# Kernel tuning notes

Measured on AMD Instinct MI355X. Metric: run time of the kernel, lower is better.

The kernel has to match this reference:

```python
import jax, jax.numpy as jnp
import numpy as np

N = 500_000          # nodes
E = 8_000_000        # edges (avg degree 16)
C = 2                # in/out channels
STEP_DIM = 8
NUM_STEPS = 100
K = 2                # k_hops -> powers [0, 1]
HID = 8              # hidden_layers


def setup_inputs() -> dict:
    key = jax.random.key(0)
    ks = jax.random.split(key, 6)
    X = jax.random.normal(ks[0], (N, C), dtype=jnp.float32)
    edge_index = jax.random.randint(ks[1], (2, E), 0, N, dtype=jnp.int32)
    step_emb = jax.random.normal(ks[2], (NUM_STEPS, STEP_DIM), dtype=jnp.float32)
    d_in0 = C + STEP_DIM  # 10
    # layer 0: one Linear per power p in {0,1}
    W0 = jax.random.normal(ks[3], (K, d_in0, C), dtype=jnp.float32) / np.sqrt(d_in0).astype(np.float32)
    b0 = jnp.zeros((K, C), dtype=jnp.float32)
    # layers 1..7, stacked for lax.scan
    Wh = jax.random.normal(ks[4], (HID - 1, K, C, C), dtype=jnp.float32) / np.sqrt(C).astype(np.float32)
    bh = jnp.zeros((HID - 1, K, C), dtype=jnp.float32)
    return dict(X=X, edge_index=edge_index, step_index=7, step_emb=step_emb,
                W0=W0, b0=b0, Wh=Wh, bh=bh)


def _make_prop(edge_index, n):
    """GCN-normalized propagation with self-loops (PyG gcn_norm), as used by MixHopConv."""
    src, dst = edge_index[0], edge_index[1]
    # in-degree on destination nodes, +1 for the self-loop
    deg = jnp.zeros((n,), jnp.float32).at[dst].add(1.0) + 1.0
    dis = jax.lax.rsqrt(deg)  # deg^{-1/2}; deg >= 1 so no inf handling needed
    edge_w = dis[src] * dis[dst]  # [E]

    def prop(x):
        msg = x[src] * edge_w[:, None]                      # [E, F] gather
        out = jax.ops.segment_sum(msg, dst, num_segments=n)  # [N, F] scatter-add
        return out + x * (dis * dis)[:, None]               # self-loop term
    return prop


def reference(X, edge_index, step_index, step_emb, W0, b0, Wh, bh):
    n = X.shape[0]
    prop = _make_prop(edge_index, n)

    s = jnp.broadcast_to(step_emb[step_index], (n, STEP_DIM))
    x = jnp.concatenate([X, s], axis=-1)  # [N, 10]

    # layer 0: concat(xW0, (Ax)W1) -> view(-1,K,C).sum(1) -> relu  ==  relu(xW0+b0 + (Ax)W1+b1)
    x = jax.nn.relu(x @ W0[0] + b0[0] + prop(x) @ W0[1] + b0[1])  # [N, 2]

    def body(x, wb):
        W, b = wb  # W: [K, C, C], b: [K, C]
        h = x @ W[0] + b[0] + prop(x) @ W[1] + b[1]
        return jax.nn.relu(h), None

    x, _ = jax.lax.scan(body, x, (Wh, bh))
    return x
```

## Files before the change

kernel.cpp:

```cpp
#include <hip/hip_runtime.h>


constexpr int NN = 500000;
constexpr int NE = 8000000;
constexpr int STEP_DIM = 8;
constexpr int HIDM1 = 7;

constexpr int BSH  = 9;
constexpr int BNOD = 1 << BSH;
constexpr int NBUK = (NN + BNOD - 1) / BNOD;
constexpr int NQ   = 4;
constexpr int SUBQ = 2560;
constexpr int SLOT = NQ * SUBQ;
constexpr int KEYS = NQ * BNOD;
constexpr unsigned SENT = (unsigned)BNOD << 19;

constexpr int PA_NBLK = 500;
constexpr int PA_EPB  = NE / PA_NBLK;
constexpr int PA_QPB  = PA_EPB / 4;
constexpr int PA_SC   = NBUK + 1;

typedef unsigned u32x4 __attribute__((ext_vector_type(4)));

__device__ __forceinline__ int swizQ(int p) {
  int w = p / 320;
  int r = p - w * 320;
  int l = r / 5;
  int o = r - l * 5;
  return w * 320 + (o < 4 ? l * 4 + o : 256 + l);
}

__device__ __forceinline__ int wave_iscan(int v, int lane) {
#pragma unroll
  for (int off = 1; off < 64; off <<= 1) {
    int n = __shfl_up(v, off, 64);
    if (lane >= off) v += n;
  }
  return v;
}


__global__ __launch_bounds__(512) void k_lsort(const int* __restrict__ src,
                                               const int* __restrict__ dst,
                                               unsigned* __restrict__ colraw,
                                               int* __restrict__ starts2) {
  __shared__ unsigned stage[PA_EPB];
  __shared__ int hist[NBUK];
  __shared__ int tsum[512];
  int b = blockIdx.x, t = threadIdx.x;
  for (int h = t; h < NBUK; h += 512) hist[h] = 0;
  __syncthreads();
  const int4* d4p = (const int4*)dst + (size_t)b * PA_QPB;
  const int4* s4p = (const int4*)src + (size_t)b * PA_QPB;
  for (int i = t; i < PA_QPB; i += 512) {
    int4 d = d4p[i];
    atomicAdd(&hist[d.x >> BSH], 1);
    atomicAdd(&hist[d.y >> BSH], 1);
    atomicAdd(&hist[d.z >> BSH], 1);
    atomicAdd(&hist[d.w >> BSH], 1);
  }
  __syncthreads();
  int h0 = 2 * t, h1 = 2 * t + 1;
  int a0 = (h0 < NBUK) ? hist[h0] : 0;
  int a1 = (h1 < NBUK) ? hist[h1] : 0;
  tsum[t] = a0 + a1;
  __syncthreads();
  for (int o = 1; o < 512; o <<= 1) {
    int v = (t >= o) ? tsum[t - o] : 0;
    __syncthreads();
    tsum[t] += v;
    __syncthreads();
  }
  int ex = tsum[t] - (a0 + a1);
  __syncthreads();
  if (h0 < NBUK) hist[h0] = ex;
  if (h1 < NBUK) hist[h1] = ex + a0;
  __syncthreads();
  int* st = starts2 + (size_t)b * PA_SC;
  for (int h = t; h < NBUK; h += 512) st[h] = hist[h];
  if (t == 0) st[NBUK] = PA_EPB;
  __syncthreads();
  for (int i = t; i < PA_QPB; i += 512) {
    int4 d = d4p[i];
    int4 s = s4p[i];
    int p0 = atomicAdd(&hist[d.x >> BSH], 1);
    stage[p0] = ((unsigned)(d.x & (BNOD - 1)) << 19) | (unsigned)s.x;
    int p1 = atomicAdd(&hist[d.y >> BSH], 1);
    stage[p1] = ((unsigned)(d.y & (BNOD - 1)) << 19) | (unsigned)s.y;
    int p2 = atomicAdd(&hist[d.z >> BSH], 1);
    stage[p2] = ((unsigned)(d.z & (BNOD - 1)) << 19) | (unsigned)s.z;
    int p3 = atomicAdd(&hist[d.w >> BSH], 1);
    stage[p3] = ((unsigned)(d.w & (BNOD - 1)) << 19) | (unsigned)s.w;
  }
  __syncthreads();
  u32x4* out4 = (u32x4*)(colraw + (size_t)b * PA_EPB);
  for (int i = t; i < PA_QPB; i += 512) {
    u32x4 q;
    q[0] = stage[4 * i + 0];
    q[1] = stage[4 * i + 1];
    q[2] = stage[4 * i + 2];
    q[3] = stage[4 * i + 3];
    __builtin_nontemporal_store(q, out4 + i);
  }
}


__global__ __launch_bounds__(512) void k_sortA(const unsigned* __restrict__ colraw,
                                               const int* __restrict__ starts2,
                                               unsigned* __restrict__ col2,
                                               const float2* __restrict__ X,
                                               const float* __restrict__ W0,
                                               const float* __restrict__ step_emb,
                                               const int* __restrict__ step_index,
                                               float* __restrict__ dis,
                                               float2* __restrict__ qtab) {
  __shared__ unsigned stage[SLOT];
  __shared__ int hist[KEYS];
  __shared__ int rp[PA_NBLK + 1];
  __shared__ int rs[PA_NBLK];
  __shared__ int wpart[8];
  __shared__ int qsh[5];
  int h = blockIdx.x, t = threadIdx.x;
  int wv = t >> 6, lane = t & 63;
  int s = 0, len = 0;
  if (t < PA_NBLK) {
    s = starts2[(size_t)t * PA_SC + h];
    len = starts2[(size_t)t * PA_SC + h + 1] - s;
  }
  hist[4 * t] = 0;
  hist[4 * t + 1] = 0;
  hist[4 * t + 2] = 0;
  hist[4 * t + 3] = 0;
  int incl = wave_iscan(len, lane);
  if (lane == 63) wpart[wv] = incl;
  __syncthreads();
  int wpre = 0, tot = 0;
#pragma unroll
  for (int k = 0; k < 8; ++k) {
    int pv = wpart[k];
    if (k < wv) wpre += pv;
    tot += pv;
  }
  int pos = wpre + incl - len;
  if (t < PA_NBLK) {
    rp[t] = pos;
    rs[t] = s;
  }
  if (t == 511) rp[PA_NBLK] = tot;
  __syncthreads();
  int ns = tot;
  if (ns > SLOT) ns = SLOT;
  {
    int g = t >> 4, gl = t & 15;
    for (int r = g; r < PA_NBLK; r += 32) {
      int P = rp[r];
      int L = rp[r + 1] - P;
      const unsigned* rw = colraw + (size_t)r * PA_EPB + rs[r];
      for (int j = gl; j < L; j += 16) {
        int p = P + j;
        if (p < SLOT) stage[p] = rw[j];
      }
    }
  }
  __syncthreads();
  for (int i = t; i < ns; i += 512)
    atomicAdd(&hist[(int)(((stage[i] >> 17) & 3u) * BNOD) + (int)(stage[i] >> 19)], 1);
  __syncthreads();
  int deg = hist[t] + hist[t + 512] + hist[t + 1024] + hist[t + 1536];
  int a0 = hist[4 * t], a1 = hist[4 * t + 1], a2 = hist[4 * t + 2], a3 = hist[4 * t + 3];
  int ssum = a0 + a1 + a2 + a3;
  int incl2 = wave_iscan(ssum, lane);
  if (lane == 63) wpart[wv] = incl2;
  __syncthreads();
  int wpre2 = 0;
#pragma unroll
  for (int k = 0; k < 8; ++k) {
    if (k < wv) wpre2 += wpart[k];
  }
  int ex = wpre2 + incl2 - ssum;
  hist[4 * t] = ex;
  hist[4 * t + 1] = ex + a0;
  hist[4 * t + 2] = ex + a0 + a1;
  hist[4 * t + 3] = ex + a0 + a1 + a2;
  if ((t & 127) == 0) qsh[t >> 7] = ex;
  if (t == 511) qsh[4] = ns;
  __syncthreads();
  unsigned* base = col2 + (size_t)h * SLOT;
  for (int i = t; i < ns; i += 512) {
    unsigned p = stage[i];
    int k = (int)(((p >> 17) & 3u) * BNOD) + (int)(p >> 19);
    int posQ = atomicAdd(&hist[k], 1) - qsh[k >> 9];
    if (posQ < SUBQ) base[(k >> 9) * SUBQ + swizQ(posQ)] = p;
  }
  for (int q = 0; q < NQ; ++q) {
    int cnt = qsh[q + 1] - qsh[q];
    if (cnt > SUBQ) cnt = SUBQ;
    if (cnt < 0) cnt = 0;
    for (int j = cnt + t; j < SUBQ; j += 512) base[q * SUBQ + swizQ(j)] = SENT;
  }
  int i = (h << BSH) + t;
  if (i < NN) {
    float d = rsqrtf((float)deg + 1.0f);
    dis[i] = d;
    float2 x = X[i];
    const float* sv = step_emb + step_index[0] * STEP_DIM;
    float c1_0 = 0.f, c1_1 = 0.f;
#pragma unroll
    for (int j = 0; j < STEP_DIM; ++j) {
      c1_0 += sv[j] * W0[20 + (2 + j) * 2 + 0];
      c1_1 += sv[j] * W0[20 + (2 + j) * 2 + 1];
    }
    qtab[i] = make_float2(d * (x.x * W0[20] + x.y * W0[22] + c1_0),
                          d * (x.x * W0[21] + x.y * W0[23] + c1_1));
  }
}


__global__ __launch_bounds__(512, 8) void k_blayer0(const unsigned int* __restrict__ col2,
                                                    const float2* __restrict__ qtab,
                                                    const float2* __restrict__ X,
                                                    const float* __restrict__ dis,
                                                    const float* __restrict__ W0,
                                                    const float* __restrict__ b0,
                                                    const float* __restrict__ step_emb,
                                                    const int* __restrict__ step_index,
                                                    float2* __restrict__ xs_out) {
  __shared__ float acc[(BNOD + 1) * 2];
  int b = blockIdx.x, t = threadIdx.x;
  for (int j = t; j < (BNOD + 1) * 2; j += 512) acc[j] = 0.f;
  __syncthreads();
  int w = t >> 6, l = t & 63;
  const unsigned* bp = col2 + (size_t)b * SLOT + w * 320;
  unsigned ebuf[NQ * 5];
#pragma unroll
  for (int q = 0; q < NQ; ++q) {
    u32x4 v = __builtin_nontemporal_load((const u32x4*)(bp + q * SUBQ + l * 4));
    ebuf[q * 5 + 0] = v[0];
    ebuf[q * 5 + 1] = v[1];
    ebuf[q * 5 + 2] = v[2];
    ebuf[q * 5 + 3] = v[3];
    ebuf[q * 5 + 4] = __builtin_nontemporal_load(bp + q * SUBQ + 256 + l);
  }
  int cur = BNOD;
  float rx = 0.f, ry = 0.f;
#pragma unroll
  for (int q = 0; q < NQ; ++q) {
    float2 vals[5];
#pragma unroll
    for (int j = 0; j < 5; ++j) vals[j] = qtab[ebuf[q * 5 + j] & 0x7FFFF];
#pragma unroll
    for (int j = 0; j < 5; ++j) {
      unsigned p = ebuf[q * 5 + j];
      int ld = (int)(p >> 19);
      if (ld != cur) {
        atomicAdd(&acc[cur * 2 + 0], rx);
        atomicAdd(&acc[cur * 2 + 1], ry);
        cur = ld;
        rx = vals[j].x; ry = vals[j].y;
      } else {
        rx += vals[j].x; ry += vals[j].y;
      }
    }
  }
  atomicAdd(&acc[cur * 2 + 0], rx);
  atomicAdd(&acc[cur * 2 + 1], ry);
  __syncthreads();
  const float* sv = step_emb + step_index[0] * STEP_DIM;
  float c00 = b0[0] + b0[2], c01 = b0[1] + b0[3];
#pragma unroll
  for (int j = 0; j < STEP_DIM; ++j) {
    c00 += sv[j] * W0[(2 + j) * 2 + 0];
    c01 += sv[j] * W0[(2 + j) * 2 + 1];
  }
  int i = (b << BSH) + t;
  if (i < NN) {
    float d = dis[i];
    float2 x = X[i];
    float2 qv = qtab[i];
    float h0 = c00 + x.x * W0[0] + x.y * W0[2] + d * (acc[t * 2 + 0] + qv.x);
    float h1 = c01 + x.x * W0[1] + x.y * W0[3] + d * (acc[t * 2 + 1] + qv.y);
    h0 = fmaxf(h0, 0.f);
    h1 = fmaxf(h1, 0.f);
    xs_out[i] = make_float2(d * h0, d * h1);
  }
}

__global__ __launch_bounds__(512, 8) void k_blayer(const unsigned int* __restrict__ col2,
                                                   const float* __restrict__ dis,
                                                   const float2* __restrict__ xs_in,
                                                   const float* __restrict__ W,
                                                   const float* __restrict__ bb,
                                                   float2* __restrict__ xs_out,
                                                   float2* __restrict__ out,
                                                   int last) {
  __shared__ float acc[(BNOD + 1) * 2];
  int b = blockIdx.x, t = threadIdx.x;
  for (int j = t; j < (BNOD + 1) * 2; j += 512) acc[j] = 0.f;
  __syncthreads();
  int w = t >> 6, l = t & 63;
  const unsigned* bp = col2 + (size_t)b * SLOT + w * 320;
  unsigned ebuf[NQ * 5];
#pragma unroll
  for (int q = 0; q < NQ; ++q) {
    u32x4 v = __builtin_nontemporal_load((const u32x4*)(bp + q * SUBQ + l * 4));
    ebuf[q * 5 + 0] = v[0];
    ebuf[q * 5 + 1] = v[1];
    ebuf[q * 5 + 2] = v[2];
    ebuf[q * 5 + 3] = v[3];
    ebuf[q * 5 + 4] = __builtin_nontemporal_load(bp + q * SUBQ + 256 + l);
  }
  int cur = BNOD;
  float rx = 0.f, ry = 0.f;
#pragma unroll
  for (int q = 0; q < NQ; ++q) {
    float2 vals[5];
#pragma unroll
    for (int j = 0; j < 5; ++j) vals[j] = xs_in[ebuf[q * 5 + j] & 0x7FFFF];
#pragma unroll
    for (int j = 0; j < 5; ++j) {
      unsigned p = ebuf[q * 5 + j];
      int ld = (int)(p >> 19);
      if (ld != cur) {
        atomicAdd(&acc[cur * 2 + 0], rx);
        atomicAdd(&acc[cur * 2 + 1], ry);
        cur = ld;
        rx = vals[j].x; ry = vals[j].y;
      } else {
        rx += vals[j].x; ry += vals[j].y;
      }
    }
  }
  atomicAdd(&acc[cur * 2 + 0], rx);
  atomicAdd(&acc[cur * 2 + 1], ry);
  __syncthreads();
  int i = (b << BSH) + t;
  if (i < NN) {
    float d = dis[i];
    float2 xsv = xs_in[i];
    float inv = 1.0f / d;
    float xx = xsv.x * inv, xy = xsv.y * inv;
    float px = d * (acc[t * 2 + 0] + xsv.x);
    float py = d * (acc[t * 2 + 1] + xsv.y);
    float h0 = bb[0] + bb[2] + xx * W[0] + xy * W[2] + px * W[4] + py * W[6];
    float h1 = bb[1] + bb[3] + xx * W[1] + xy * W[3] + px * W[5] + py * W[7];
    h0 = fmaxf(h0, 0.f);
    h1 = fmaxf(h1, 0.f);
    if (last) {
      out[i] = make_float2(h0, h1);
    } else {
      xs_out[i] = make_float2(d * h0, d * h1);
    }
  }
}


extern "C" void kernel_launch(void* const* d_in, const int* in_sizes, int n_in,
                              void* d_out, int out_size, void* d_ws, size_t ws_size,
                              hipStream_t stream) {
  const float2* X        = (const float2*)d_in[0];
  const int*    edge     = (const int*)d_in[1];
  const int*    src      = edge;
  const int*    dstp     = edge + NE;
  const int*    step_idx = (const int*)d_in[2];
  const float*  step_emb = (const float*)d_in[3];
  const float*  W0       = (const float*)d_in[4];
  const float*  b0       = (const float*)d_in[5];
  const float*  Wh       = (const float*)d_in[6];
  const float*  bbias    = (const float*)d_in[7];

  int*      ip      = (int*)d_ws;
  unsigned* col2    = (unsigned*)ip;
  size_t    o       = (size_t)NBUK * SLOT;
  unsigned* colraw  = (unsigned*)(ip + o);  o += NE;
  int*      starts2 = ip + o;               o += ((size_t)PA_NBLK * PA_SC + 8) & ~(size_t)3;
  float*    dis     = (float*)(ip + o);     o += 500224;
  float2*   bufA    = (float2*)(ip + o);    o += 2 * 500224;
  float2*   bufB    = (float2*)(ip + o);

  k_lsort<<<PA_NBLK, 512, 0, stream>>>(src, dstp, colraw, starts2);
  k_sortA<<<NBUK, 512, 0, stream>>>(colraw, starts2, col2, X, W0,
                                    step_emb, step_idx, dis, bufA);

  k_blayer0<<<NBUK, 512, 0, stream>>>(col2, bufA, X, dis, W0, b0,
                                      step_emb, step_idx, bufB);
  float2* cur = bufB;
  float2* nxt = bufA;
  for (int l = 0; l < HIDM1; ++l) {
    k_blayer<<<NBUK, 512, 0, stream>>>(col2, dis, cur, Wh + l * 8,
                                       bbias + l * 4, nxt, (float2*)d_out,
                                       l == HIDM1 - 1 ? 1 : 0);
    float2* tmp = cur;
    cur = nxt;
    nxt = tmp;
  }
}
```

Measured before the change: 555.4 us.

## Fuse all propagation layers into one cooperative kernel with register-resident edges

Replaces the eight per-layer launches with a single cooperative kernel that loads each block's edge list into registers once and reuses it across all layers, using grid-wide syncs between layers. It also removes the four-way subqueue split in the bucket sort and moves to a single-key counting sort with a new swizzled layout giving fully vectorised 16-byte loads. This avoids re-reading the edge array every layer and cuts launch gaps. In exchange it needs all 977 blocks of 512 threads resident at once, otherwise it falls back to the old path. Grid syncs add their own barrier cost.

```diff
diff --git a/kernel.cpp b/kernel.cpp
--- a/kernel.cpp
+++ b/kernel.cpp
@@ -1,4 +1,7 @@
 #include <hip/hip_runtime.h>
+#include <hip/hip_cooperative_groups.h>
+
+namespace cg = cooperative_groups;
 
 
 constexpr int NN = 500000;
@@ -9,10 +12,8 @@
 constexpr int BSH  = 9;
 constexpr int BNOD = 1 << BSH;
 constexpr int NBUK = (NN + BNOD - 1) / BNOD;
-constexpr int NQ   = 4;
-constexpr int SUBQ = 2560;
-constexpr int SLOT = NQ * SUBQ;
-constexpr int KEYS = NQ * BNOD;
+constexpr int SLOT = 10240;
+constexpr int WSLOT = 1280;
 constexpr unsigned SENT = (unsigned)BNOD << 19;
 
 constexpr int PA_NBLK = 500;
@@ -22,12 +23,12 @@
 
 typedef unsigned u32x4 __attribute__((ext_vector_type(4)));
 
-__device__ __forceinline__ int swizQ(int p) {
-  int w = p / 320;
-  int r = p - w * 320;
-  int l = r / 5;
-  int o = r - l * 5;
-  return w * 320 + (o < 4 ? l * 4 + o : 256 + l);
+__device__ __forceinline__ int swiz(int p) {
+  int w = p / WSLOT;
+  int r = p - w * WSLOT;
+  int tid = r / 20;
+  int j = r - tid * 20;
+  return w * WSLOT + ((j >> 2) << 8) + (tid << 2) + (j & 3);
 }
 
 __device__ __forceinline__ int wave_iscan(int v, int lane) {
@@ -115,11 +116,10 @@
                                                float* __restrict__ dis,
                                                float2* __restrict__ qtab) {
   __shared__ unsigned stage[SLOT];
-  __shared__ int hist[KEYS];
+  __shared__ int hist[BNOD];
   __shared__ int rp[PA_NBLK + 1];
   __shared__ int rs[PA_NBLK];
   __shared__ int wpart[8];
-  __shared__ int qsh[5];
   int h = blockIdx.x, t = threadIdx.x;
   int wv = t >> 6, lane = t & 63;
   int s = 0, len = 0;
@@ -127,10 +127,7 @@
     s = starts2[(size_t)t * PA_SC + h];
     len = starts2[(size_t)t * PA_SC + h + 1] - s;
   }
-  hist[4 * t] = 0;
-  hist[4 * t + 1] = 0;
-  hist[4 * t + 2] = 0;
-  hist[4 * t + 3] = 0;
+  hist[t] = 0;
   int incl = wave_iscan(len, lane);
   if (lane == 63) wpart[wv] = incl;
   __syncthreads();
@@ -164,12 +161,10 @@
   }
   __syncthreads();
   for (int i = t; i < ns; i += 512)
-    atomicAdd(&hist[(int)(((stage[i] >> 17) & 3u) * BNOD) + (int)(stage[i] >> 19)], 1);
-  __syncthreads();
-  int deg = hist[t] + hist[t + 512] + hist[t + 1024] + hist[t + 1536];
-  int a0 = hist[4 * t], a1 = hist[4 * t + 1], a2 = hist[4 * t + 2], a3 = hist[4 * t + 3];
-  int ssum = a0 + a1 + a2 + a3;
-  int incl2 = wave_iscan(ssum, lane);
+    atomicAdd(&hist[stage[i] >> 19], 1);
+  __syncthreads();
+  int deg = hist[t];
+  int incl2 = wave_iscan(deg, lane);
   if (lane == 63) wpart[wv] = incl2;
   __syncthreads();
   int wpre2 = 0;
@@ -177,27 +172,15 @@
   for (int k = 0; k < 8; ++k) {
     if (k < wv) wpre2 += wpart[k];
   }
-  int ex = wpre2 + incl2 - ssum;
-  hist[4 * t] = ex;
-  hist[4 * t + 1] = ex + a0;
-  hist[4 * t + 2] = ex + a0 + a1;
-  hist[4 * t + 3] = ex + a0 + a1 + a2;
-  if ((t & 127) == 0) qsh[t >> 7] = ex;
-  if (t == 511) qsh[4] = ns;
+  hist[t] = wpre2 + incl2 - deg;
   __syncthreads();
   unsigned* base = col2 + (size_t)h * SLOT;
   for (int i = t; i < ns; i += 512) {
     unsigned p = stage[i];
-    int k = (int)(((p >> 17) & 3u) * BNOD) + (int)(p >> 19);
-    int posQ = atomicAdd(&hist[k], 1) - qsh[k >> 9];
-    if (posQ < SUBQ) base[(k >> 9) * SUBQ + swizQ(posQ)] = p;
-  }
-  for (int q = 0; q < NQ; ++q) {
-    int cnt = qsh[q + 1] - qsh[q];
-    if (cnt > SUBQ) cnt = SUBQ;
-    if (cnt < 0) cnt = 0;
-    for (int j = cnt + t; j < SUBQ; j += 512) base[q * SUBQ + swizQ(j)] = SENT;
-  }
+    int posQ = atomicAdd(&hist[(int)(p >> 19)], 1);
+    if (posQ < SLOT) base[swiz(posQ)] = p;
+  }
+  for (int j = ns + t; j < SLOT; j += 512) base[swiz(j)] = SENT;
   int i = (h << BSH) + t;
   if (i < NN) {
     float d = rsqrtf((float)deg + 1.0f);
@@ -216,7 +199,128 @@
 }
 
 
-__global__ __launch_bounds__(512, 8) void k_blayer0(const unsigned int* __restrict__ col2,
+__device__ __forceinline__ void load_ebuf(const unsigned* __restrict__ col2,
+                                          int b, int w, int l, unsigned* ebuf) {
+  const unsigned* bp = col2 + (size_t)b * SLOT + w * WSLOT + l * 4;
+#pragma unroll
+  for (int g = 0; g < 5; ++g) {
+    u32x4 v = __builtin_nontemporal_load((const u32x4*)(bp + g * 256));
+    ebuf[g * 4 + 0] = v[0];
+    ebuf[g * 4 + 1] = v[1];
+    ebuf[g * 4 + 2] = v[2];
+    ebuf[g * 4 + 3] = v[3];
+  }
+}
+
+__device__ __forceinline__ void gather_acc(const unsigned* ebuf,
+                                           const float2* tab, float* acc) {
+  int cur = BNOD;
+  float rx = 0.f, ry = 0.f;
+#pragma unroll
+  for (int g = 0; g < 5; ++g) {
+    float2 vals[4];
+#pragma unroll
+    for (int r = 0; r < 4; ++r) vals[r] = tab[ebuf[g * 4 + r] & 0x7FFFF];
+#pragma unroll
+    for (int r = 0; r < 4; ++r) {
+      int ld = (int)(ebuf[g * 4 + r] >> 19);
+      if (ld != cur) {
+        atomicAdd(&acc[cur * 2 + 0], rx);
+        atomicAdd(&acc[cur * 2 + 1], ry);
+        cur = ld;
+        rx = vals[r].x;
+        ry = vals[r].y;
+      } else {
+        rx += vals[r].x;
+        ry += vals[r].y;
+      }
+    }
+  }
+  atomicAdd(&acc[cur * 2 + 0], rx);
+  atomicAdd(&acc[cur * 2 + 1], ry);
+}
+
+
+__global__ __launch_bounds__(512, 8) void k_layers(
+    const unsigned* __restrict__ col2,
+    float2* qtab,
+    const float2* __restrict__ X,
+    const float* __restrict__ dis,
+    const float* __restrict__ W0,
+    const float* __restrict__ b0,
+    const float* __restrict__ step_emb,
+    const int* __restrict__ step_index,
+    const float* __restrict__ Wh,
+    const float* __restrict__ bh,
+    float2* bufB,
+    float2* out) {
+  cg::grid_group grid = cg::this_grid();
+  __shared__ float acc[(BNOD + 1) * 2];
+  int b = blockIdx.x, t = threadIdx.x;
+  int w = t >> 6, l = t & 63;
+  unsigned ebuf[20];
+  load_ebuf(col2, b, w, l, ebuf);
+  int i = (b << BSH) + t;
+  bool act = i < NN;
+  float d = dis[i];
+  float inv = 1.0f / d;
+  for (int j = t; j < (BNOD + 1) * 2; j += 512) acc[j] = 0.f;
+  __syncthreads();
+  gather_acc(ebuf, (const float2*)qtab, acc);
+  __syncthreads();
+  const float* sv = step_emb + step_index[0] * STEP_DIM;
+  float c00 = b0[0] + b0[2], c01 = b0[1] + b0[3];
+#pragma unroll
+  for (int j = 0; j < STEP_DIM; ++j) {
+    c00 += sv[j] * W0[(2 + j) * 2 + 0];
+    c01 += sv[j] * W0[(2 + j) * 2 + 1];
+  }
+  float2 xsv = make_float2(0.f, 0.f);
+  if (act) {
+    float2 x = X[i];
+    float2 qv = qtab[i];
+    float h0 = c00 + x.x * W0[0] + x.y * W0[2] + d * (acc[t * 2 + 0] + qv.x);
+    float h1 = c01 + x.x * W0[1] + x.y * W0[3] + d * (acc[t * 2 + 1] + qv.y);
+    h0 = fmaxf(h0, 0.f);
+    h1 = fmaxf(h1, 0.f);
+    xsv = make_float2(d * h0, d * h1);
+    bufB[i] = xsv;
+  }
+  grid.sync();
+  float2* curb = bufB;
+  float2* nxtb = qtab;
+#pragma unroll 1
+  for (int L = 0; L < HIDM1; ++L) {
+    for (int j = t; j < (BNOD + 1) * 2; j += 512) acc[j] = 0.f;
+    __syncthreads();
+    gather_acc(ebuf, (const float2*)curb, acc);
+    __syncthreads();
+    const float* W = Wh + L * 8;
+    const float* bb = bh + L * 4;
+    if (act) {
+      float px = d * (acc[t * 2 + 0] + xsv.x);
+      float py = d * (acc[t * 2 + 1] + xsv.y);
+      float xx = xsv.x * inv, xy = xsv.y * inv;
+      float h0 = bb[0] + bb[2] + xx * W[0] + xy * W[2] + px * W[4] + py * W[6];
+      float h1 = bb[1] + bb[3] + xx * W[1] + xy * W[3] + px * W[5] + py * W[7];
+      h0 = fmaxf(h0, 0.f);
+      h1 = fmaxf(h1, 0.f);
+      if (L == HIDM1 - 1) {
+        out[i] = make_float2(h0, h1);
+      } else {
+        xsv = make_float2(d * h0, d * h1);
+        nxtb[i] = xsv;
+      }
+    }
+    if (L != HIDM1 - 1) grid.sync();
+    float2* tmp = curb;
+    curb = nxtb;
+    nxtb = tmp;
+  }
+}
+
+
+__global__ __launch_bounds__(512, 8) void k_blayer0(const unsigned* __restrict__ col2,
                                                     const float2* __restrict__ qtab,
                                                     const float2* __restrict__ X,
                                                     const float* __restrict__ dis,
@@ -230,40 +334,9 @@
   for (int j = t; j < (BNOD + 1) * 2; j += 512) acc[j] = 0.f;
   __syncthreads();
   int w = t >> 6, l = t & 63;
-  const unsigned* bp = col2 + (size_t)b * SLOT + w * 320;
-  unsigned ebuf[NQ * 5];
-#pragma unroll
-  for (int q = 0; q < NQ; ++q) {
-    u32x4 v = __builtin_nontemporal_load((const u32x4*)(bp + q * SUBQ + l * 4));
-    ebuf[q * 5 + 0] = v[0];
-    ebuf[q * 5 + 1] = v[1];
-    ebuf[q * 5 + 2] = v[2];
-    ebuf[q * 5 + 3] = v[3];
-    ebuf[q * 5 + 4] = __builtin_nontemporal_load(bp + q * SUBQ + 256 + l);
-  }
-  int cur = BNOD;
-  float rx = 0.f, ry = 0.f;
-#pragma unroll
-  for (int q = 0; q < NQ; ++q) {
-    float2 vals[5];
-#pragma unroll
-    for (int j = 0; j < 5; ++j) vals[j] = qtab[ebuf[q * 5 + j] & 0x7FFFF];
-#pragma unroll
-    for (int j = 0; j < 5; ++j) {
-      unsigned p = ebuf[q * 5 + j];
-      int ld = (int)(p >> 19);
-      if (ld != cur) {
-        atomicAdd(&acc[cur * 2 + 0], rx);
-        atomicAdd(&acc[cur * 2 + 1], ry);
-        cur = ld;
-        rx = vals[j].x; ry = vals[j].y;
-      } else {
-        rx += vals[j].x; ry += vals[j].y;
-      }
-    }
-  }
-  atomicAdd(&acc[cur * 2 + 0], rx);
-  atomicAdd(&acc[cur * 2 + 1], ry);
+  unsigned ebuf[20];
+  load_ebuf(col2, b, w, l, ebuf);
+  gather_acc(ebuf, qtab, acc);
   __syncthreads();
   const float* sv = step_emb + step_index[0] * STEP_DIM;
   float c00 = b0[0] + b0[2], c01 = b0[1] + b0[3];
@@ -285,7 +358,7 @@
   }
 }
 
-__global__ __launch_bounds__(512, 8) void k_blayer(const unsigned int* __restrict__ col2,
+__global__ __launch_bounds__(512, 8) void k_blayer(const unsigned* __restrict__ col2,
                                                    const float* __restrict__ dis,
                                                    const float2* __restrict__ xs_in,
                                                    const float* __restrict__ W,
@@ -298,40 +371,9 @@
   for (int j = t; j < (BNOD + 1) * 2; j += 512) acc[j] = 0.f;
   __syncthreads();
   int w = t >> 6, l = t & 63;
-  const unsigned* bp = col2 + (size_t)b * SLOT + w * 320;
-  unsigned ebuf[NQ * 5];
-#pragma unroll
-  for (int q = 0; q < NQ; ++q) {
-    u32x4 v = __builtin_nontemporal_load((const u32x4*)(bp + q * SUBQ + l * 4));
-    ebuf[q * 5 + 0] = v[0];
-    ebuf[q * 5 + 1] = v[1];
-    ebuf[q * 5 + 2] = v[2];
-    ebuf[q * 5 + 3] = v[3];
-    ebuf[q * 5 + 4] = __builtin_nontemporal_load(bp + q * SUBQ + 256 + l);
-  }
-  int cur = BNOD;
-  float rx = 0.f, ry = 0.f;
-#pragma unroll
-  for (int q = 0; q < NQ; ++q) {
-    float2 vals[5];
-#pragma unroll
-    for (int j = 0; j < 5; ++j) vals[j] = xs_in[ebuf[q * 5 + j] & 0x7FFFF];
-#pragma unroll
-    for (int j = 0; j < 5; ++j) {
-      unsigned p = ebuf[q * 5 + j];
-      int ld = (int)(p >> 19);
-      if (ld != cur) {
-        atomicAdd(&acc[cur * 2 + 0], rx);
-        atomicAdd(&acc[cur * 2 + 1], ry);
-        cur = ld;
-        rx = vals[j].x; ry = vals[j].y;
-      } else {
-        rx += vals[j].x; ry += vals[j].y;
-      }
-    }
-  }
-  atomicAdd(&acc[cur * 2 + 0], rx);
-  atomicAdd(&acc[cur * 2 + 1], ry);
+  unsigned ebuf[20];
+  load_ebuf(col2, b, w, l, ebuf);
+  gather_acc(ebuf, xs_in, acc);
   __syncthreads();
   int i = (b << BSH) + t;
   if (i < NN) {
@@ -381,16 +423,35 @@
   k_sortA<<<NBUK, 512, 0, stream>>>(colraw, starts2, col2, X, W0,
                                     step_emb, step_idx, dis, bufA);
 
-  k_blayer0<<<NBUK, 512, 0, stream>>>(col2, bufA, X, dis, W0, b0,
-                                      step_emb, step_idx, bufB);
-  float2* cur = bufB;
-  float2* nxt = bufA;
-  for (int l = 0; l < HIDM1; ++l) {
-    k_blayer<<<NBUK, 512, 0, stream>>>(col2, dis, cur, Wh + l * 8,
-                                       bbias + l * 4, nxt, (float2*)d_out,
-                                       l == HIDM1 - 1 ? 1 : 0);
-    float2* tmp = cur;
-    cur = nxt;
-    nxt = tmp;
-  }
-}
+  const unsigned* a_col2 = col2;
+  float2*         a_qtab = bufA;
+  const float2*   a_X    = X;
+  const float*    a_dis  = dis;
+  const float*    a_W0   = W0;
+  const float*    a_b0   = b0;
+  const float*    a_se   = step_emb;
+  const int*      a_si   = step_idx;
+  const float*    a_Wh   = Wh;
+  const float*    a_bh   = bbias;
+  float2*         a_bufB = bufB;
+  float2*         a_out  = (float2*)d_out;
+  void* cargs[] = {&a_col2, &a_qtab, &a_X, &a_dis, &a_W0, &a_b0,
+                   &a_se,   &a_si,   &a_Wh, &a_bh, &a_bufB, &a_out};
+  hipError_t ce = hipLaunchCooperativeKernel(k_layers, dim3(NBUK), dim3(512),
+                                             cargs, 0, stream);
+  if (ce != hipSuccess) {
+    (void)hipGetLastError();
+    k_blayer0<<<NBUK, 512, 0, stream>>>(col2, bufA, X, dis, W0, b0,
+                                        step_emb, step_idx, bufB);
+    float2* cur = bufB;
+    float2* nxt = bufA;
+    for (int l = 0; l < HIDM1; ++l) {
+      k_blayer<<<NBUK, 512, 0, stream>>>(col2, dis, cur, Wh + l * 8,
+                                         bbias + l * 4, nxt, (float2*)d_out,
+                                         l == HIDM1 - 1 ? 1 : 0);
+      float2* tmp = cur;
+      cur = nxt;
+      nxt = tmp;
+    }
+  }
+}
```

After: 1.562 ms. 181% more time.
